# Kernel tuning notes

Measured on AMD Instinct MI355X. Metric: run time of the kernel, lower is better.

## Reference

```python
import itertools
import jax, jax.numpy as jnp
import numpy as np

G = 128          # grid points per dimension
D_IN = 3         # domain dimension
D_OUT = 16       # codomain dimension
N_QUERY = 1 << 20


def setup_inputs() -> dict:
    key = jax.random.key(0)
    kx, ky = jax.random.split(key)
    # Sorted, non-uniform grid coordinates in [0, 1] per dimension
    base = jnp.linspace(0.0, 1.0, G, dtype=jnp.float32)
    xs0 = base
    xs1 = base ** 1.5            # non-uniform spacing, still sorted
    xs2 = jnp.sqrt(base)         # non-uniform spacing, still sorted
    # Vector-valued samples on the tensor grid
    y = jax.random.normal(ky, (G, G, G, D_OUT), dtype=jnp.float32)
    # Query points, slightly outside [0,1] to exercise clamped extension
    x = jax.random.uniform(kx, (N_QUERY, D_IN), dtype=jnp.float32,
                           minval=-0.1, maxval=1.1)
    return {"x": x, "y": y, "xs0": xs0, "xs1": xs1, "xs2": xs2}


def _interp_linear_clamped(x, y, xs):
    """Multilinear interpolation of grid function y (G,...,G,D) at x (N,d_in),
    clamped extension. Faithful to _grid_interpolate(method='linear',
    extend='clamped')."""
    d_in = len(xs)
    x_min = jnp.stack([g[0] for g in xs])   # (d_in,)
    x_max = jnp.stack([g[-1] for g in xs])  # (d_in,)
    xq = jnp.clip(x, x_min[None], x_max[None])  # clamp to domain

    left, ts = [], []
    for i, g in enumerate(xs):
        n = g.shape[0]
        # index of left grid point: searchsorted right, minus 1
        li = jnp.searchsorted(g, xq[:, i], side="right") - 1
        # points exactly at the upper boundary belong to the last cell
        li = jnp.where(xq[:, i] == g[-1], li - 1, li)
        li = jnp.clip(li, 0, n - 2)  # after clamping all queries are internal
        t = (xq[:, i] - g[li]) / (g[li + 1] - g[li])  # fractional coordinate
        left.append(li)
        ts.append(t)

    # Accumulate over the 2^d_in cell corners
    result = jnp.zeros((x.shape[0], y.shape[-1]), dtype=y.dtype)
    for exponent in itertools.product((0, 1), repeat=d_in):
        c = jnp.ones_like(ts[0])
        for i in range(d_in):
            c = c * (ts[i] if exponent[i] else 1.0 - ts[i])
        idx = tuple(left[i] + exponent[i] for i in range(d_in))
        val = y[idx]  # (N, D_OUT) gather of corner values
        result = result + c[:, None] * val
    return result


def reference(x, y, xs0, xs1, xs2):
    return _interp_linear_clamped(x, y, [xs0, xs1, xs2])
```

## Files before the change

kernel.cpp:

```cpp
#include <hip/hip_runtime.h>

#define G 128
#define D_OUT 16
#define BIN_SHIFT 3
#define NBINS (16 * 16 * 16)
#define NBLK 256

typedef float f32x4 __attribute__((ext_vector_type(4)));


__device__ __forceinline__ void stage_grids(const float* __restrict__ xs0,
                                            const float* __restrict__ xs1,
                                            const float* __restrict__ xs2,
                                            float (*sxs)[G], int tid, int nthreads)
{
    for (int i = tid; i < 3 * G; i += nthreads) {
        float v;
        if (i < G)            v = xs0[i];
        else if (i < 2 * G)   v = xs1[i - G];
        else                  v = xs2[i - 2 * G];
        (&sxs[0][0])[i] = v;
    }
}

__device__ __forceinline__ void search1(const float* __restrict__ g, float v,
                                        int& li, float& t)
{
    v = fminf(fmaxf(v, g[0]), g[G - 1]);
    int idx = 0;
    #pragma unroll
    for (int s = 64; s >= 1; s >>= 1) {
        int cand = idx + s;
        if (g[cand] <= v) idx = cand;
    }
    if (idx > G - 2) idx = G - 2;
    li = idx;
    t  = (v - g[idx]) / (g[idx + 1] - g[idx]);
}

__device__ __forceinline__ int bin_of(int li0, int li1, int li2)
{
    return ((li0 >> BIN_SHIFT) << 8) | ((li1 >> BIN_SHIFT) << 4) | (li2 >> BIN_SHIFT);
}


__global__ __launch_bounds__(256) void hist_kernel(
    const float* __restrict__ x,
    const float* __restrict__ xs0, const float* __restrict__ xs1, const float* __restrict__ xs2,
    unsigned int* __restrict__ counts,
    int n, int qpb)
{
    __shared__ float sxs[3][G];
    __shared__ unsigned int hist[NBINS];
    const int tid = threadIdx.x, blk = blockIdx.x;

    stage_grids(xs0, xs1, xs2, sxs, tid, 256);
    for (int i = tid; i < NBINS; i += 256) hist[i] = 0u;
    __syncthreads();

    const int q0 = blk * qpb, q1 = min(n, q0 + qpb);
    for (int q = q0 + tid; q < q1; q += 256) {
        int li[3]; float t;
        #pragma unroll
        for (int d = 0; d < 3; ++d) search1(sxs[d], x[q * 3 + d], li[d], t);
        atomicAdd(&hist[bin_of(li[0], li[1], li[2])], 1u);
    }
    __syncthreads();

    for (int i = tid; i < NBINS; i += 256)
        counts[(size_t)blk * NBINS + i] = hist[i];
}


__global__ __launch_bounds__(256) void scan_block_kernel(
    const unsigned int* __restrict__ counts,
    unsigned int* __restrict__ offs,
    unsigned int* __restrict__ totals)
{
    __shared__ unsigned int sd[NBLK];
    const int b = blockIdx.x, k = threadIdx.x;
    const unsigned int v = counts[(size_t)k * NBINS + b];
    sd[k] = v;
    __syncthreads();
    for (int off = 1; off < NBLK; off <<= 1) {
        unsigned int t = sd[k];
        unsigned int a = (k >= off) ? sd[k - off] : 0u;
        __syncthreads();
        sd[k] = t + a;
        __syncthreads();
    }
    const unsigned int incl = sd[k];
    offs[(size_t)k * NBINS + b] = incl - v;
    if (k == NBLK - 1) totals[b] = incl;
}


__global__ __launch_bounds__(1024) void scan_totals_kernel(
    const unsigned int* __restrict__ totals, unsigned int* __restrict__ bin_base)
{
    __shared__ unsigned int sd[1024];
    const int t = threadIdx.x;
    uint4 c = ((const uint4*)totals)[t];
    unsigned int s = c.x + c.y + c.z + c.w;
    sd[t] = s;
    __syncthreads();
    for (int off = 1; off < 1024; off <<= 1) {
        unsigned int v = sd[t];
        unsigned int add = (t >= off) ? sd[t - off] : 0u;
        __syncthreads();
        sd[t] = v + add;
        __syncthreads();
    }
    unsigned int excl = sd[t] - s;
    uint4 o;
    o.x = excl;
    o.y = o.x + c.x;
    o.z = o.y + c.y;
    o.w = o.z + c.z;
    ((uint4*)bin_base)[t] = o;
}


__global__ __launch_bounds__(256) void scatter_kernel(
    const float* __restrict__ x,
    const float* __restrict__ xs0, const float* __restrict__ xs1, const float* __restrict__ xs2,
    const unsigned int* __restrict__ offs,
    const unsigned int* __restrict__ bin_base,
    float4* __restrict__ payload,
    unsigned int* __restrict__ cells,
    int n, int qpb)
{
    __shared__ float sxs[3][G];
    __shared__ unsigned int base[NBINS];
    const int tid = threadIdx.x, blk = blockIdx.x;

    stage_grids(xs0, xs1, xs2, sxs, tid, 256);
    for (int i = tid; i < NBINS; i += 256)
        base[i] = bin_base[i] + offs[(size_t)blk * NBINS + i];
    __syncthreads();

    const int q0 = blk * qpb, q1 = min(n, q0 + qpb);
    for (int q = q0 + tid; q < q1; q += 256) {
        int li0, li1, li2; float t0, t1, t2;
        search1(sxs[0], x[q * 3 + 0], li0, t0);
        search1(sxs[1], x[q * 3 + 1], li1, t1);
        search1(sxs[2], x[q * 3 + 2], li2, t2);
        unsigned int slot = atomicAdd(&base[bin_of(li0, li1, li2)], 1u);
        payload[slot] = make_float4(t0, t1, t2, __uint_as_float((unsigned int)q));
        cells[slot]   = ((unsigned int)li0 << 14) | ((unsigned int)li1 << 7) | (unsigned int)li2;
    }
}


__global__ __launch_bounds__(256) void interp_gather_kernel(
    const float4* __restrict__ payload,
    const unsigned int* __restrict__ cells,
    const float* __restrict__ y,
    float* __restrict__ out, int n)
{
    int bid = blockIdx.x;
    int nb  = gridDim.x;
    if ((nb & 7) == 0) {
        int chunk = nb >> 3;
        bid = (bid & 7) * chunk + (bid >> 3);
    }

    const int i = bid * 64 + (threadIdx.x >> 2);
    if (i >= n) return;
    const int cg = (threadIdx.x & 3) * 4;

    const float4 p = payload[i];
    const unsigned int cell = cells[i];
    const unsigned int q = __float_as_uint(p.w);

    const float t0 = p.x, t1 = p.y, t2 = p.z;
    const float u0 = 1.f - t0, u1 = 1.f - t1, u2 = 1.f - t2;

    const float* yb = y + (size_t)cell * D_OUT + cg;
    const f32x4 v000 = *(const f32x4*)(yb);
    const f32x4 v001 = *(const f32x4*)(yb + D_OUT);
    const f32x4 v010 = *(const f32x4*)(yb + G * D_OUT);
    const f32x4 v011 = *(const f32x4*)(yb + G * D_OUT + D_OUT);
    const f32x4 v100 = *(const f32x4*)(yb + G * G * D_OUT);
    const f32x4 v101 = *(const f32x4*)(yb + G * G * D_OUT + D_OUT);
    const f32x4 v110 = *(const f32x4*)(yb + G * G * D_OUT + G * D_OUT);
    const f32x4 v111 = *(const f32x4*)(yb + G * G * D_OUT + G * D_OUT + D_OUT);

    const float w000 = u0 * u1 * u2, w001 = u0 * u1 * t2;
    const float w010 = u0 * t1 * u2, w011 = u0 * t1 * t2;
    const float w100 = t0 * u1 * u2, w101 = t0 * u1 * t2;
    const float w110 = t0 * t1 * u2, w111 = t0 * t1 * t2;

    f32x4 acc = w000 * v000 + w001 * v001 + w010 * v010 + w011 * v011
              + w100 * v100 + w101 * v101 + w110 * v110 + w111 * v111;

    __builtin_nontemporal_store(acc, (f32x4*)(out + (size_t)q * D_OUT + cg));
}


__global__ __launch_bounds__(256) void interp3d_kernel(
    const float* __restrict__ x, const float* __restrict__ y,
    const float* __restrict__ xs0, const float* __restrict__ xs1, const float* __restrict__ xs2,
    float* __restrict__ out, int nquery)
{
    __shared__ float sxs[3][G];
    stage_grids(xs0, xs1, xs2, sxs, threadIdx.x, 256);
    __syncthreads();

    const int q = blockIdx.x * 64 + (threadIdx.x >> 2);
    if (q >= nquery) return;
    const int cg = (threadIdx.x & 3) * 4;

    int li[3]; float t[3];
    #pragma unroll
    for (int d = 0; d < 3; ++d) search1(sxs[d], x[q * 3 + d], li[d], t[d]);

    const float w0[3] = { 1.f - t[0], 1.f - t[1], 1.f - t[2] };
    const float w1[3] = { t[0], t[1], t[2] };

    float4 acc = make_float4(0.f, 0.f, 0.f, 0.f);
    #pragma unroll
    for (int e = 0; e < 8; ++e) {
        const int e0 = (e >> 2) & 1, e1 = (e >> 1) & 1, e2 = e & 1;
        const float w = (e0 ? w1[0] : w0[0]) * (e1 ? w1[1] : w0[1]) * (e2 ? w1[2] : w0[2]);
        const int idx = ((li[0] + e0) * G + (li[1] + e1)) * G + (li[2] + e2);
        const float4 v = *(const float4*)(y + (size_t)idx * D_OUT + cg);
        acc.x += w * v.x; acc.y += w * v.y; acc.z += w * v.z; acc.w += w * v.w;
    }
    *(float4*)(out + (size_t)q * D_OUT + cg) = acc;
}

extern "C" void kernel_launch(void* const* d_in, const int* in_sizes, int n_in,
                              void* d_out, int out_size, void* d_ws, size_t ws_size,
                              hipStream_t stream) {
    const float* x   = (const float*)d_in[0];
    const float* y   = (const float*)d_in[1];
    const float* xs0 = (const float*)d_in[2];
    const float* xs1 = (const float*)d_in[3];
    const float* xs2 = (const float*)d_in[4];
    float* out = (float*)d_out;

    const int nquery = in_sizes[0] / 3;

    const size_t counts_elems = (size_t)NBLK * NBINS;
    const size_t need = (2 * counts_elems + 2 * NBINS) * sizeof(unsigned int)
                      + (size_t)nquery * (sizeof(float4) + sizeof(unsigned int));
    if (ws_size < need) {
        const int blocks = (nquery + 63) / 64;
        hipLaunchKernelGGL(interp3d_kernel, dim3(blocks), dim3(256), 0, stream,
                           x, y, xs0, xs1, xs2, out, nquery);
        return;
    }

    unsigned int* counts   = (unsigned int*)d_ws;
    unsigned int* offs     = counts + counts_elems;
    unsigned int* totals   = offs + counts_elems;
    unsigned int* bin_base = totals + NBINS;
    float4*       payload  = (float4*)(bin_base + NBINS);
    unsigned int* cells    = (unsigned int*)(payload + nquery);

    const int qpb = (nquery + NBLK - 1) / NBLK;

    hipLaunchKernelGGL(hist_kernel, dim3(NBLK), dim3(256), 0, stream,
                       x, xs0, xs1, xs2, counts, nquery, qpb);
    hipLaunchKernelGGL(scan_block_kernel, dim3(NBINS), dim3(NBLK), 0, stream,
                       counts, offs, totals);
    hipLaunchKernelGGL(scan_totals_kernel, dim3(1), dim3(1024), 0, stream,
                       totals, bin_base);
    hipLaunchKernelGGL(scatter_kernel, dim3(NBLK), dim3(256), 0, stream,
                       x, xs0, xs1, xs2, offs, bin_base, payload, cells, nquery, qpb);

    const int b64 = (nquery + 63) / 64;
    hipLaunchKernelGGL(interp_gather_kernel, dim3(b64), dim3(256), 0, stream,
                       payload, cells, y, out, nquery);
}
```

Measured before the change: 100.8 us.

## Stage per-bin grid region in LDS and interpolate bin chunks from shared memory

Replaces the per-query global gather of eight corner vectors with a chunked kernel. Each block loads the 9x9x9x16 grid region covering one spatial bin into shared memory, then interpolates up to 1024 sorted queries of that bin from LDS. Local cell offsets are packed into the payload word, so the separate cells array is dropped. The scan kernel now also builds a chunk-to-bin map. The costs are a redundant halo load per chunk, a serial map-building loop, a fixed 5120-block grid, and a query index limited to 20 bits.

Measured after the change: 118.9 us. 1.18x slower.

```diff
diff --git a/kernel.cpp b/kernel.cpp
--- a/kernel.cpp
+++ b/kernel.cpp
@@ -5,6 +5,8 @@
 #define BIN_SHIFT 3
 #define NBINS (16 * 16 * 16)
 #define NBLK 256
+#define QPB 1024
+#define MAXCHUNK 5120
 
 typedef float f32x4 __attribute__((ext_vector_type(4)));
 
@@ -96,28 +98,54 @@
 
 
 __global__ __launch_bounds__(1024) void scan_totals_kernel(
-    const unsigned int* __restrict__ totals, unsigned int* __restrict__ bin_base)
-{
-    __shared__ unsigned int sd[1024];
+    const unsigned int* __restrict__ totals,
+    unsigned int* __restrict__ bin_base,
+    unsigned int* __restrict__ map,
+    unsigned int* __restrict__ nchunks)
+{
+    __shared__ unsigned int sq[1024], sc[1024];
     const int t = threadIdx.x;
     uint4 c = ((const uint4*)totals)[t];
-    unsigned int s = c.x + c.y + c.z + c.w;
-    sd[t] = s;
+    uint4 h;
+    h.x = (c.x + QPB - 1) / QPB;
+    h.y = (c.y + QPB - 1) / QPB;
+    h.z = (c.z + QPB - 1) / QPB;
+    h.w = (c.w + QPB - 1) / QPB;
+    const unsigned int sum_q = c.x + c.y + c.z + c.w;
+    const unsigned int sum_c = h.x + h.y + h.z + h.w;
+    sq[t] = sum_q; sc[t] = sum_c;
     __syncthreads();
     for (int off = 1; off < 1024; off <<= 1) {
-        unsigned int v = sd[t];
-        unsigned int add = (t >= off) ? sd[t - off] : 0u;
+        unsigned int vq = sq[t], vc = sc[t];
+        unsigned int aq = (t >= off) ? sq[t - off] : 0u;
+        unsigned int ac = (t >= off) ? sc[t - off] : 0u;
         __syncthreads();
-        sd[t] = v + add;
+        sq[t] = vq + aq; sc[t] = vc + ac;
         __syncthreads();
     }
-    unsigned int excl = sd[t] - s;
-    uint4 o;
-    o.x = excl;
-    o.y = o.x + c.x;
-    o.z = o.y + c.y;
-    o.w = o.z + c.z;
-    ((uint4*)bin_base)[t] = o;
+    const unsigned int eq = sq[t] - sum_q;
+    const unsigned int ec = sc[t] - sum_c;
+
+    uint4 qb;
+    qb.x = eq;
+    qb.y = qb.x + c.x;
+    qb.z = qb.y + c.y;
+    qb.w = qb.z + c.z;
+    ((uint4*)bin_base)[t] = qb;
+    if (t == 1023) {
+        bin_base[NBINS] = sq[1023];
+        nchunks[0] = sc[1023];
+    }
+
+    unsigned int cb = ec;
+    unsigned int hh[4] = { h.x, h.y, h.z, h.w };
+    #pragma unroll
+    for (int k = 0; k < 4; ++k) {
+        const unsigned int binid = ((unsigned int)t << 2) | k;
+        for (unsigned int j = 0; j < hh[k]; ++j)
+            map[cb + j] = (binid << 8) | j;
+        cb += hh[k];
+    }
 }
 
 
@@ -127,7 +155,6 @@
     const unsigned int* __restrict__ offs,
     const unsigned int* __restrict__ bin_base,
     float4* __restrict__ payload,
-    unsigned int* __restrict__ cells,
     int n, int qpb)
 {
     __shared__ float sxs[3][G];
@@ -146,55 +173,89 @@
         search1(sxs[1], x[q * 3 + 1], li1, t1);
         search1(sxs[2], x[q * 3 + 2], li2, t2);
         unsigned int slot = atomicAdd(&base[bin_of(li0, li1, li2)], 1u);
-        payload[slot] = make_float4(t0, t1, t2, __uint_as_float((unsigned int)q));
-        cells[slot]   = ((unsigned int)li0 << 14) | ((unsigned int)li1 << 7) | (unsigned int)li2;
-    }
-}
-
-
-__global__ __launch_bounds__(256) void interp_gather_kernel(
+        const unsigned int bits = ((unsigned int)(li0 & 7) << 26)
+                                | ((unsigned int)(li1 & 7) << 23)
+                                | ((unsigned int)(li2 & 7) << 20)
+                                | (unsigned int)q;
+        payload[slot] = make_float4(t0, t1, t2, __uint_as_float(bits));
+    }
+}
+
+
+__global__ __launch_bounds__(256) void interp_staged_kernel(
     const float4* __restrict__ payload,
-    const unsigned int* __restrict__ cells,
     const float* __restrict__ y,
-    float* __restrict__ out, int n)
-{
+    const unsigned int* __restrict__ bin_base,
+    const unsigned int* __restrict__ map,
+    const unsigned int* __restrict__ nchunks,
+    float* __restrict__ out)
+{
+    __shared__ float region[9 * 9 * 9 * D_OUT];
+    const int tid = threadIdx.x;
+
     int bid = blockIdx.x;
-    int nb  = gridDim.x;
-    if ((nb & 7) == 0) {
-        int chunk = nb >> 3;
+    {
+        const int chunk = MAXCHUNK >> 3;
         bid = (bid & 7) * chunk + (bid >> 3);
     }
-
-    const int i = bid * 64 + (threadIdx.x >> 2);
-    if (i >= n) return;
-    const int cg = (threadIdx.x & 3) * 4;
-
-    const float4 p = payload[i];
-    const unsigned int cell = cells[i];
-    const unsigned int q = __float_as_uint(p.w);
-
-    const float t0 = p.x, t1 = p.y, t2 = p.z;
-    const float u0 = 1.f - t0, u1 = 1.f - t1, u2 = 1.f - t2;
-
-    const float* yb = y + (size_t)cell * D_OUT + cg;
-    const f32x4 v000 = *(const f32x4*)(yb);
-    const f32x4 v001 = *(const f32x4*)(yb + D_OUT);
-    const f32x4 v010 = *(const f32x4*)(yb + G * D_OUT);
-    const f32x4 v011 = *(const f32x4*)(yb + G * D_OUT + D_OUT);
-    const f32x4 v100 = *(const f32x4*)(yb + G * G * D_OUT);
-    const f32x4 v101 = *(const f32x4*)(yb + G * G * D_OUT + D_OUT);
-    const f32x4 v110 = *(const f32x4*)(yb + G * G * D_OUT + G * D_OUT);
-    const f32x4 v111 = *(const f32x4*)(yb + G * G * D_OUT + G * D_OUT + D_OUT);
-
-    const float w000 = u0 * u1 * u2, w001 = u0 * u1 * t2;
-    const float w010 = u0 * t1 * u2, w011 = u0 * t1 * t2;
-    const float w100 = t0 * u1 * u2, w101 = t0 * u1 * t2;
-    const float w110 = t0 * t1 * u2, w111 = t0 * t1 * t2;
-
-    f32x4 acc = w000 * v000 + w001 * v001 + w010 * v010 + w011 * v011
-              + w100 * v100 + w101 * v101 + w110 * v110 + w111 * v111;
-
-    __builtin_nontemporal_store(acc, (f32x4*)(out + (size_t)q * D_OUT + cg));
+    if ((unsigned int)bid >= nchunks[0]) return;
+
+    const unsigned int info = map[bid];
+    const unsigned int bin  = info >> 8;
+    const unsigned int chk  = info & 255u;
+    const int o0 = (int)((bin >> 8) & 15u) << 3;
+    const int o1 = (int)((bin >> 4) & 15u) << 3;
+    const int o2 = (int)(bin & 15u) << 3;
+
+    for (int s = tid; s < 81 * 36; s += 256) {
+        const int row = s / 36;
+        const int f4  = s - row * 36;
+        const int l0 = row / 9, l1 = row - l0 * 9;
+        const int cc = f4 >> 2, ch = f4 & 3;
+        const int g0 = min(o0 + l0, G - 1);
+        const int g1 = min(o1 + l1, G - 1);
+        const int g2 = min(o2 + cc, G - 1);
+        const f32x4 v = *(const f32x4*)(y + ((((g0 << 7) | g1) << 7) | g2) * D_OUT + (ch << 2));
+        *(f32x4*)&region[((l0 * 9 + l1) * 9 + cc) * D_OUT + (ch << 2)] = v;
+    }
+    __syncthreads();
+
+    const unsigned int qs = bin_base[bin] + chk * QPB;
+    const unsigned int qe = min(bin_base[bin + 1], qs + QPB);
+    const int cg = (tid & 3) << 2;
+
+    for (unsigned int i = qs + (tid >> 2); i < qe; i += 64) {
+        const float4 p = payload[i];
+        const unsigned int bits = __float_as_uint(p.w);
+        const unsigned int q   = bits & 0xFFFFFu;
+        const unsigned int lc0 = (bits >> 26) & 7u;
+        const unsigned int lc1 = (bits >> 23) & 7u;
+        const unsigned int lc2 = (bits >> 20) & 7u;
+
+        const float t0 = p.x, t1 = p.y, t2 = p.z;
+        const float u0 = 1.f - t0, u1 = 1.f - t1, u2 = 1.f - t2;
+
+        const int base = (int)((lc0 * 9u + lc1) * 9u + lc2) * D_OUT + cg;
+        const int d2 = D_OUT, d1 = 9 * D_OUT, d0 = 81 * D_OUT;
+        const f32x4 v000 = *(const f32x4*)&region[base];
+        const f32x4 v001 = *(const f32x4*)&region[base + d2];
+        const f32x4 v010 = *(const f32x4*)&region[base + d1];
+        const f32x4 v011 = *(const f32x4*)&region[base + d1 + d2];
+        const f32x4 v100 = *(const f32x4*)&region[base + d0];
+        const f32x4 v101 = *(const f32x4*)&region[base + d0 + d2];
+        const f32x4 v110 = *(const f32x4*)&region[base + d0 + d1];
+        const f32x4 v111 = *(const f32x4*)&region[base + d0 + d1 + d2];
+
+        const float w000 = u0 * u1 * u2, w001 = u0 * u1 * t2;
+        const float w010 = u0 * t1 * u2, w011 = u0 * t1 * t2;
+        const float w100 = t0 * u1 * u2, w101 = t0 * u1 * t2;
+        const float w110 = t0 * t1 * u2, w111 = t0 * t1 * t2;
+
+        f32x4 acc = w000 * v000 + w001 * v001 + w010 * v010 + w011 * v011
+                  + w100 * v100 + w101 * v101 + w110 * v110 + w111 * v111;
+
+        __builtin_nontemporal_store(acc, (f32x4*)(out + (size_t)q * D_OUT + cg));
+    }
 }
 
 
@@ -243,21 +304,22 @@
     const int nquery = in_sizes[0] / 3;
 
     const size_t counts_elems = (size_t)NBLK * NBINS;
-    const size_t need = (2 * counts_elems + 2 * NBINS) * sizeof(unsigned int)
-                      + (size_t)nquery * (sizeof(float4) + sizeof(unsigned int));
-    if (ws_size < need) {
+    const size_t need = (size_t)nquery * sizeof(float4)
+                      + (2 * counts_elems + NBINS + (NBINS + 1) + MAXCHUNK + 16) * sizeof(unsigned int);
+    if (ws_size < need || nquery > (1 << 20)) {
         const int blocks = (nquery + 63) / 64;
         hipLaunchKernelGGL(interp3d_kernel, dim3(blocks), dim3(256), 0, stream,
                            x, y, xs0, xs1, xs2, out, nquery);
         return;
     }
 
-    unsigned int* counts   = (unsigned int*)d_ws;
+    float4*       payload  = (float4*)d_ws;
+    unsigned int* counts   = (unsigned int*)(payload + nquery);
     unsigned int* offs     = counts + counts_elems;
     unsigned int* totals   = offs + counts_elems;
     unsigned int* bin_base = totals + NBINS;
-    float4*       payload  = (float4*)(bin_base + NBINS);
-    unsigned int* cells    = (unsigned int*)(payload + nquery);
+    unsigned int* map      = bin_base + (NBINS + 1);
+    unsigned int* nchunks  = map + MAXCHUNK;
 
     const int qpb = (nquery + NBLK - 1) / NBLK;
 
@@ -266,11 +328,9 @@
     hipLaunchKernelGGL(scan_block_kernel, dim3(NBINS), dim3(NBLK), 0, stream,
                        counts, offs, totals);
     hipLaunchKernelGGL(scan_totals_kernel, dim3(1), dim3(1024), 0, stream,
-                       totals, bin_base);
+                       totals, bin_base, map, nchunks);
     hipLaunchKernelGGL(scatter_kernel, dim3(NBLK), dim3(256), 0, stream,
-                       x, xs0, xs1, xs2, offs, bin_base, payload, cells, nquery, qpb);
-
-    const int b64 = (nquery + 63) / 64;
-    hipLaunchKernelGGL(interp_gather_kernel, dim3(b64), dim3(256), 0, stream,
-                       payload, cells, y, out, nquery);
-}
+                       x, xs0, xs1, xs2, offs, bin_base, payload, nquery, qpb);
+    hipLaunchKernelGGL(interp_staged_kernel, dim3(MAXCHUNK), dim3(256), 0, stream,
+                       payload, y, bin_base, map, nchunks, out);
+}
```
